# Performance work log

Measured on AMD Instinct MI355X. Metric: run time of the kernel, lower is better.

## Reference

```python
import jax, jax.numpy as jnp
import numpy as np

B, F, T, D, O = 8192, 512, 64, 6, 128
N_INTERNAL = 2 ** D - 1  # 63
N_LEAVES = 2 ** D        # 64


def smooth_step(t):
    tc = jnp.clip(t, -0.5, 0.5)
    return -2.0 * tc ** 3 + 1.5 * tc + 0.5


def setup_inputs() -> dict:
    key = jax.random.key(0)
    k1, k2, k3, k4 = jax.random.split(key, 4)
    x = jax.random.normal(k1, (B, F), dtype=jnp.float32)
    # Stacked per-node Linear weights in BFS (heap) order: node i -> row i.
    W_nodes = jax.random.normal(k2, (N_INTERNAL, F, T), dtype=jnp.float32) * (1.0 / np.sqrt(F))
    b_nodes = jax.random.normal(k3, (N_INTERNAL, T), dtype=jnp.float32) * 0.01
    # Per-leaf mixing weight [out_features, num_trees], leaves in BFS order.
    W_leaf = jax.random.normal(k4, (N_LEAVES, O, T), dtype=jnp.float32)
    return {"x": x, "W_nodes": W_nodes, "b_nodes": b_nodes, "W_leaf": W_leaf}


def reference(x, W_nodes, b_nodes, W_leaf):
    n_internal = W_nodes.shape[0]
    depth = int(np.log2(n_internal + 1))
    # All internal-node gates in one stacked GEMM: [B, n_internal, T]
    s = smooth_step(jnp.einsum('bf,nft->bnt', x, W_nodes) + b_nodes[None, :, :])
    b, _, t = s.shape
    prob = jnp.ones((b, 1, t), dtype=s.dtype)  # root prob
    start = 0
    for lvl in range(depth):
        width = 2 ** lvl
        s_l = s[:, start:start + width]  # [B, width, T], nodes at this level
        start += width
        # node local j -> children local 2j (left, prob*s) and 2j+1 (right, prob*(1-s))
        prob = jnp.stack([prob * s_l, prob * (1.0 - s_l)], axis=2).reshape(b, 2 * width, t)
    # prob: [B, n_leaves, T]; mix per-leaf, per-tree weights -> [B, O]
    out = jnp.einsum('blt,lot->bo', prob, W_leaf)
    return out
```

## Files before the change

### kernel.cpp

```cpp
#include <hip/hip_runtime.h>
#include <hip/hip_fp16.h>

#define BATCH 8192
#define FDIM  512
#define NTREE 64
#define NODES 63
#define ODIM  128
#define NJP   4096
#define K2    4096
#define TPG   8

typedef _Float16 f16;
typedef _Float16 f16x2 __attribute__((ext_vector_type(2)));
typedef _Float16 f16x4 __attribute__((ext_vector_type(4)));
typedef _Float16 f16x8 __attribute__((ext_vector_type(8)));
typedef float    f32x4 __attribute__((ext_vector_type(4)));

#define XH_OFF   0
#define XH_SZ    ((size_t)BATCH*FDIM*2)
#define WNH_OFF  (XH_OFF + XH_SZ)
#define WNH_SZ   ((size_t)NJP*FDIM*2)
#define WLT_OFF  (WNH_OFF + WNH_SZ)
#define WLT_SZ   ((size_t)ODIM*K2*2)
#define PS_OFF   (WLT_OFF + WLT_SZ)
#define PS_SZ    ((size_t)TPG*BATCH*ODIM*4)
#define WS_NEEDED (PS_OFF + PS_SZ)

__device__ __forceinline__ float smooth_step_f(float t) {
    float tc = fminf(fmaxf(t, -0.5f), 0.5f);
    return fmaf(tc, fmaf(-2.0f * tc, tc, 1.5f), 0.5f);
}

__device__ __forceinline__ int sw_off(int row, int g) {
    return ((row >> 3) * 512) + (((row & 7) * 8 + (g ^ (row & 7))) * 8);
}

__global__ __launch_bounds__(256)
void prep_kernel(const float* __restrict__ x, const float* __restrict__ wn,
                 const float* __restrict__ wl,
                 f16* __restrict__ xf, f16* __restrict__ wnf, f16* __restrict__ wlf)
{
    const int bid = blockIdx.x, tid = threadIdx.x;
    if (bid < 512) {
        const int bx = bid >> 3, k0 = bid & 7;
        f16* dst = xf + ((size_t)bx * 8192 + (size_t)k0 * 1024) * 8;
        #pragma unroll
        for (int c = 0; c < 4; ++c) {
            int fid  = c * 256 + tid;
            int lane = fid & 63, ks = (fid >> 6) & 1, tm = (fid >> 7) & 3, wm = (fid >> 9) & 1;
            int row  = bx * 128 + wm * 64 + tm * 16 + (lane & 15);
            int k    = k0 * 64 + (ks * 4 + (lane >> 4)) * 8;
            const float* s = x + (size_t)row * FDIM + k;
            float4 a = *(const float4*)s, b = *(const float4*)(s + 4);
            f16x8 v = { (f16)a.x, (f16)a.y, (f16)a.z, (f16)a.w,
                        (f16)b.x, (f16)b.y, (f16)b.z, (f16)b.w };
            *(f16x8*)(dst + (size_t)fid * 8) = v;
        }
    } else if (bid < 768) {
        const int id = bid - 512, tp = id >> 3, k0 = id & 7;
        f16* dst = wnf + ((size_t)tp * 8192 + (size_t)k0 * 1024) * 8;
        #pragma unroll
        for (int c = 0; c < 4; ++c) {
            int fid  = c * 256 + tid;
            int lane = fid & 63, ks = (fid >> 6) & 1, tn = (fid >> 7) & 3, wq = (fid >> 9) & 1;
            int col  = tp * 128 + wq * 64 + tn * 16 + (lane & 15);
            int t    = col >> 6, n = col & 63;
            int k    = k0 * 64 + (ks * 4 + (lane >> 4)) * 8;
            f16x8 v;
            if (n == NODES) {
                #pragma unroll
                for (int e = 0; e < 8; ++e) v[e] = (f16)0.0f;
            } else {
                const float* s = wn + ((size_t)n * FDIM + k) * NTREE + t;
                #pragma unroll
                for (int e = 0; e < 8; ++e) v[e] = (f16)s[(size_t)e * NTREE];
            }
            *(f16x8*)(dst + (size_t)fid * 8) = v;
        }
    } else {
        const int tp = bid - 768;
        f16* dst = wlf + (size_t)tp * 2048 * 8;
        #pragma unroll
        for (int c = 0; c < 8; ++c) {
            int fid  = c * 256 + tid;
            int lane = fid & 63, ks = (fid >> 6) & 1, tn = (fid >> 7) & 3, wq = (fid >> 9) & 1;
            int h    = (fid >> 10) & 1;
            int o    = wq * 64 + tn * 16 + (lane & 15);
            int t    = tp * 2 + h;
            int l0   = (ks * 4 + (lane >> 4)) * 8;
            const float* s = wl + ((size_t)l0 * ODIM + o) * NTREE + t;
            f16x8 v;
            #pragma unroll
            for (int e = 0; e < 8; ++e) v[e] = (f16)s[(size_t)e * ODIM * NTREE];
            *(f16x8*)(dst + (size_t)fid * 8) = v;
        }
    }
}

__global__ __launch_bounds__(256, 2)
void fused_tree(const f16* __restrict__ xhF, const f16* __restrict__ wnhF,
                const float* __restrict__ bn, const f16* __restrict__ wltF,
                float* __restrict__ partial)
{
    __shared__ __align__(16) f16 SH[16640];
    const int tid  = threadIdx.x;
    const int lane = tid & 63;
    const int w    = tid >> 6;
    const int wm   = w & 1;
    const int wq   = w >> 1;
    const int row0 = blockIdx.x * 128;
    const int tpg  = blockIdx.y;

    const int frow = tid & 127;
    const int ftr  = tid >> 7;

    const f16x8* __restrict__ xv = (const f16x8*)xhF;
    const f16x8* __restrict__ wv = (const f16x8*)wnhF;
    const f16x8* __restrict__ lv = (const f16x8*)wltF;
    const size_t xb = (size_t)blockIdx.x * 8192 + (size_t)wm * 512 + lane;

    f32x4 lacc[4][4] = {};

    for (int tpi = 0; tpi < 4; ++tpi) {
        const int tp = tpg * 4 + tpi;
        const int j0 = tp * 128;

        const size_t wb = (size_t)tp * 8192 + (size_t)wq * 512 + lane;
        f32x4 acc[4][4] = {};
        #pragma unroll 2
        for (int k0 = 0; k0 < 8; ++k0) {
            #pragma unroll
            for (int ks = 0; ks < 2; ++ks) {
                f16x8 bfr[4];
                #pragma unroll
                for (int tn = 0; tn < 4; ++tn)
                    bfr[tn] = wv[wb + k0 * 1024 + tn * 128 + ks * 64];
                #pragma unroll
                for (int tm = 0; tm < 4; ++tm) {
                    f16x8 afr = xv[xb + k0 * 1024 + tm * 128 + ks * 64];
                    #pragma unroll
                    for (int tn = 0; tn < 4; ++tn)
                        acc[tm][tn] = __builtin_amdgcn_mfma_f32_16x16x32_f16(afr, bfr[tn], acc[tm][tn], 0, 0, 0);
                }
            }
        }

        #pragma unroll
        for (int tn = 0; tn < 4; ++tn) {
            int col = wq * 64 + tn * 16 + (lane & 15);
            int nn  = col & 63;
            int tt  = (j0 + col) >> 6;
            float bias = (nn < NODES) ? bn[nn * NTREE + tt] : 0.0f;
            #pragma unroll
            for (int tm = 0; tm < 4; ++tm) {
                #pragma unroll
                for (int r = 0; r < 4; ++r) {
                    int row = wm * 64 + tm * 16 + (lane >> 4) * 4 + r;
                    SH[row * 130 + col] = (f16)smooth_step_f(acc[tm][tn][r] + bias);
                }
            }
        }
        __syncthreads();

        f16x8 ov[8];
        {
            const f16* gp = &SH[frow * 130 + ftr * 64];
            float gg[64];
            #pragma unroll
            for (int c = 0; c < 32; ++c) {
                f16x2 v = *(const f16x2*)(gp + 2 * c);
                gg[2 * c]     = (float)v[0];
                gg[2 * c + 1] = (float)v[1];
            }
            __syncthreads();
            float pr[32];
            pr[0] = 1.0f;
            int bse = 0;
            #pragma unroll
            for (int lvl = 0; lvl < 5; ++lvl) {
                const int width = 1 << lvl;
                #pragma unroll
                for (int i = width - 1; i >= 0; --i) {
                    float p = pr[i], s = gg[bse + i];
                    pr[2 * i]     = p * s;
                    pr[2 * i + 1] = p * (1.0f - s);
                }
                bse += width;
            }
            #pragma unroll
            for (int i = 0; i < 32; ++i) {
                float s5 = gg[31 + i];
                float p  = pr[i];
                ov[i >> 2][(i & 3) * 2]     = (f16)(p * s5);
                ov[i >> 2][(i & 3) * 2 + 1] = (f16)(p * (1.0f - s5));
            }
        }

        #pragma unroll
        for (int g2 = 0; g2 < 8; ++g2)
            *(f16x8*)&SH[ftr * 8192 + sw_off(frow, g2)] = ov[g2];
        __syncthreads();

        const size_t lb = (size_t)tp * 2048 + (size_t)wq * 512 + lane;
        #pragma unroll
        for (int h = 0; h < 2; ++h) {
            #pragma unroll
            for (int ks = 0; ks < 2; ++ks) {
                int g = ks * 4 + (lane >> 4);
                f16x8 bfr[4];
                #pragma unroll
                for (int tn = 0; tn < 4; ++tn)
                    bfr[tn] = lv[lb + h * 1024 + tn * 128 + ks * 64];
                #pragma unroll
                for (int tm = 0; tm < 4; ++tm) {
                    int m = wm * 64 + tm * 16 + (lane & 15);
                    f16x8 afr = *(const f16x8*)&SH[h * 8192 + sw_off(m, g)];
                    #pragma unroll
                    for (int tn = 0; tn < 4; ++tn)
                        lacc[tm][tn] = __builtin_amdgcn_mfma_f32_16x16x32_f16(afr, bfr[tn], lacc[tm][tn], 0, 0, 0);
                }
            }
        }
        __syncthreads();
    }

    float* dst = partial + (size_t)tpg * BATCH * ODIM;
    #pragma unroll
    for (int tn = 0; tn < 4; ++tn) {
        int o = wq * 64 + tn * 16 + (lane & 15);
        #pragma unroll
        for (int tm = 0; tm < 4; ++tm) {
            #pragma unroll
            for (int r = 0; r < 4; ++r) {
                int row = row0 + wm * 64 + tm * 16 + (lane >> 4) * 4 + r;
                dst[(size_t)row * ODIM + o] = lacc[tm][tn][r];
            }
        }
    }
}

__global__ void reduce_kernel(const float* __restrict__ partial, float* __restrict__ out) {
    size_t i = ((size_t)blockIdx.x * blockDim.x + threadIdx.x) * 4;
    f32x4 a = *(const f32x4*)(partial + i);
    #pragma unroll
    for (int k = 1; k < TPG; ++k)
        a += *(const f32x4*)(partial + (size_t)k * BATCH * ODIM + i);
    *(f32x4*)(out + i) = a;
}

#define ROWS 8
__global__ __launch_bounds__(256, 2)
void soft_tree_fallback(const float* __restrict__ x, const float* __restrict__ Wn,
                        const float* __restrict__ bn, const float* __restrict__ Wl,
                        float* __restrict__ out)
{
    __shared__ __half s_lds[ROWS][NODES][NTREE];
    const int lane = threadIdx.x & 63;
    const int w    = threadIdx.x >> 6;
    const long row0 = (long)blockIdx.x * ROWS;
    for (int n = w; n < NODES; n += 4) {
        const float* wp = Wn + ((long)n * FDIM) * NTREE + lane;
        const float* xp = x + row0 * FDIM;
        float acc[ROWS];
        #pragma unroll
        for (int r = 0; r < ROWS; ++r) acc[r] = 0.0f;
        #pragma unroll 8
        for (int f = 0; f < FDIM; ++f) {
            float wv = wp[(long)f * NTREE];
            #pragma unroll
            for (int r = 0; r < ROWS; ++r)
                acc[r] = fmaf(xp[r * FDIM + f], wv, acc[r]);
        }
        float bias = bn[n * NTREE + lane];
        #pragma unroll
        for (int r = 0; r < ROWS; ++r)
            s_lds[r][n][lane] = __float2half(smooth_step_f(acc[r] + bias));
    }
    __syncthreads();
    const int r0 = w * 2, r1 = w * 2 + 1;
    float pr0[64], pr1[64];
    {
        pr0[0] = 1.0f; pr1[0] = 1.0f;
        int base = 0;
        #pragma unroll
        for (int lvl = 0; lvl < 6; ++lvl) {
            const int width = 1 << lvl;
            #pragma unroll
            for (int i = width - 1; i >= 0; --i) {
                float sa = __half2float(s_lds[r0][base + i][lane]);
                float sb = __half2float(s_lds[r1][base + i][lane]);
                float pa = pr0[i], pb = pr1[i];
                pr0[2 * i] = pa * sa; pr0[2 * i + 1] = pa * (1.0f - sa);
                pr1[2 * i] = pb * sb; pr1[2 * i + 1] = pb * (1.0f - sb);
            }
            base += width;
        }
    }
    for (int o = 0; o < ODIM; ++o) {
        const float* wlp = Wl + (long)o * NTREE + lane;
        float c0 = 0.0f, c1 = 0.0f;
        #pragma unroll
        for (int l = 0; l < 64; ++l) {
            float wv = wlp[(long)l * (ODIM * NTREE)];
            c0 = fmaf(pr0[l], wv, c0);
            c1 = fmaf(pr1[l], wv, c1);
        }
        #pragma unroll
        for (int off = 32; off > 0; off >>= 1) {
            c0 += __shfl_xor(c0, off, 64);
            c1 += __shfl_xor(c1, off, 64);
        }
        if (lane == 0) {
            out[(row0 + r0) * ODIM + o] = c0;
            out[(row0 + r1) * ODIM + o] = c1;
        }
    }
}

extern "C" void kernel_launch(void* const* d_in, const int* in_sizes, int n_in,
                              void* d_out, int out_size, void* d_ws, size_t ws_size,
                              hipStream_t stream) {
    const float* x  = (const float*)d_in[0];
    const float* Wn = (const float*)d_in[1];
    const float* bn = (const float*)d_in[2];
    const float* Wl = (const float*)d_in[3];
    float* out = (float*)d_out;

    if (ws_size < WS_NEEDED) {
        soft_tree_fallback<<<BATCH / ROWS, 256, 0, stream>>>(x, Wn, bn, Wl, out);
        return;
    }

    f16*   xh  = (f16*)((char*)d_ws + XH_OFF);
    f16*   wnh = (f16*)((char*)d_ws + WNH_OFF);
    f16*   wlt = (f16*)((char*)d_ws + WLT_OFF);
    float* ps  = (float*)((char*)d_ws + PS_OFF);

    prep_kernel<<<800, 256, 0, stream>>>(x, Wn, Wl, xh, wnh, wlt);
    fused_tree<<<dim3(BATCH / 128, TPG), 256, 0, stream>>>(xh, wnh, bn, wlt, ps);
    reduce_kernel<<<(BATCH * ODIM) / (256 * 4), 256, 0, stream>>>(ps, out);
}
```

Baseline: 161.8 us.

## Halve fused tree block rows, split leaf-prob work, coalesce weight prep reads

The fused tree kernel now handles 64 batch rows per block instead of 128, which halves the accumulator registers and raises launch bounds to four blocks per CU. That doubles the grid and gives more parallelism. The leaf-probability stage is split so two threads share each row-tree pair, each computing half the subtree and reading gates straight from shared memory. The gates and leaf tiles are kept in separate LDS regions, so one barrier is dropped. Prep kernels for the node and leaf weights now read float4 along the tree dimension for coalesced loads, with a changed block count, at the cost of reloading node weights twice as often across the doubled grid.

```diff
diff --git a/kernel.cpp b/kernel.cpp
--- a/kernel.cpp
+++ b/kernel.cpp
@@ -47,8 +47,8 @@
         #pragma unroll
         for (int c = 0; c < 4; ++c) {
             int fid  = c * 256 + tid;
-            int lane = fid & 63, ks = (fid >> 6) & 1, tm = (fid >> 7) & 3, wm = (fid >> 9) & 1;
-            int row  = bx * 128 + wm * 64 + tm * 16 + (lane & 15);
+            int lane = fid & 63, ks = (fid >> 6) & 1, rg = (fid >> 7) & 7;
+            int row  = bx * 128 + rg * 16 + (lane & 15);
             int k    = k0 * 64 + (ks * 4 + (lane >> 4)) * 8;
             const float* s = x + (size_t)row * FDIM + k;
             float4 a = *(const float4*)s, b = *(const float4*)(s + 4);
@@ -57,76 +57,89 @@
             *(f16x8*)(dst + (size_t)fid * 8) = v;
         }
     } else if (bid < 768) {
-        const int id = bid - 512, tp = id >> 3, k0 = id & 7;
-        f16* dst = wnf + ((size_t)tp * 8192 + (size_t)k0 * 1024) * 8;
-        #pragma unroll
-        for (int c = 0; c < 4; ++c) {
-            int fid  = c * 256 + tid;
-            int lane = fid & 63, ks = (fid >> 6) & 1, tn = (fid >> 7) & 3, wq = (fid >> 9) & 1;
-            int col  = tp * 128 + wq * 64 + tn * 16 + (lane & 15);
-            int t    = col >> 6, n = col & 63;
-            int k    = k0 * 64 + (ks * 4 + (lane >> 4)) * 8;
+        const int id = bid - 512;
+        const int t0 = (id >> 4) * 4;
+        const int n  = tid & 63;
+        const int k8 = (id & 15) * 4 + (tid >> 6);
+        float4 q[8];
+        if (n != NODES) {
+            #pragma unroll
+            for (int e = 0; e < 8; ++e)
+                q[e] = *(const float4*)(wn + ((size_t)n * FDIM + k8 * 8 + e) * NTREE + t0);
+        }
+        #pragma unroll
+        for (int j = 0; j < 4; ++j) {
+            int t  = t0 + j;
+            int tp = t >> 1;
+            int cg = (t & 1) * 4 + (n >> 4);
+            size_t chunk = (size_t)tp * 8192 + (size_t)(k8 >> 3) * 1024 + cg * 128
+                         + ((k8 >> 2) & 1) * 64 + (k8 & 3) * 16 + (n & 15);
             f16x8 v;
             if (n == NODES) {
                 #pragma unroll
                 for (int e = 0; e < 8; ++e) v[e] = (f16)0.0f;
             } else {
-                const float* s = wn + ((size_t)n * FDIM + k) * NTREE + t;
-                #pragma unroll
-                for (int e = 0; e < 8; ++e) v[e] = (f16)s[(size_t)e * NTREE];
-            }
-            *(f16x8*)(dst + (size_t)fid * 8) = v;
+                const float* qf = (const float*)q;
+                #pragma unroll
+                for (int e = 0; e < 8; ++e) v[e] = (f16)qf[e * 4 + j];
+            }
+            *(f16x8*)(wnf + chunk * 8) = v;
         }
     } else {
-        const int tp = bid - 768;
-        f16* dst = wlf + (size_t)tp * 2048 * 8;
-        #pragma unroll
-        for (int c = 0; c < 8; ++c) {
-            int fid  = c * 256 + tid;
-            int lane = fid & 63, ks = (fid >> 6) & 1, tn = (fid >> 7) & 3, wq = (fid >> 9) & 1;
-            int h    = (fid >> 10) & 1;
-            int o    = wq * 64 + tn * 16 + (lane & 15);
-            int t    = tp * 2 + h;
-            int l0   = (ks * 4 + (lane >> 4)) * 8;
-            const float* s = wl + ((size_t)l0 * ODIM + o) * NTREE + t;
+        const int id = bid - 768;
+        const int t0 = (id >> 2) * 4;
+        const int o  = tid & 127;
+        const int l8 = (id & 3) * 2 + (tid >> 7);
+        float4 q[8];
+        #pragma unroll
+        for (int e = 0; e < 8; ++e)
+            q[e] = *(const float4*)(wl + ((size_t)(l8 * 8 + e) * ODIM + o) * NTREE + t0);
+        #pragma unroll
+        for (int j = 0; j < 4; ++j) {
+            int t  = t0 + j;
+            int tp = t >> 1, h = t & 1;
+            size_t chunk = (size_t)tp * 2048 + (size_t)h * 1024 + (o >> 4) * 128
+                         + (l8 >> 2) * 64 + (l8 & 3) * 16 + (o & 15);
+            const float* qf = (const float*)q;
             f16x8 v;
             #pragma unroll
-            for (int e = 0; e < 8; ++e) v[e] = (f16)s[(size_t)e * ODIM * NTREE];
-            *(f16x8*)(dst + (size_t)fid * 8) = v;
-        }
-    }
-}
-
-__global__ __launch_bounds__(256, 2)
+            for (int e = 0; e < 8; ++e) v[e] = (f16)qf[e * 4 + j];
+            *(f16x8*)(wlf + chunk * 8) = v;
+        }
+    }
+}
+
+__global__ __launch_bounds__(256, 4)
 void fused_tree(const f16* __restrict__ xhF, const f16* __restrict__ wnhF,
                 const float* __restrict__ bn, const f16* __restrict__ wltF,
                 float* __restrict__ partial)
 {
-    __shared__ __align__(16) f16 SH[16640];
+    __shared__ __align__(16) f16 SH[16512];
     const int tid  = threadIdx.x;
     const int lane = tid & 63;
     const int w    = tid >> 6;
     const int wm   = w & 1;
     const int wq   = w >> 1;
-    const int row0 = blockIdx.x * 128;
     const int tpg  = blockIdx.y;
 
-    const int frow = tid & 127;
-    const int ftr  = tid >> 7;
+    const int frow = tid & 63;
+    const int ftr  = (tid >> 6) & 1;
+    const int sub  = tid >> 7;
 
     const f16x8* __restrict__ xv = (const f16x8*)xhF;
     const f16x8* __restrict__ wv = (const f16x8*)wnhF;
     const f16x8* __restrict__ lv = (const f16x8*)wltF;
-    const size_t xb = (size_t)blockIdx.x * 8192 + (size_t)wm * 512 + lane;
-
-    f32x4 lacc[4][4] = {};
+    const size_t xb = (size_t)(blockIdx.x >> 1) * 8192
+                    + (size_t)((blockIdx.x & 1) * 4 + wm * 2) * 128 + lane;
+
+    f32x4 lacc[2][4] = {};
 
     for (int tpi = 0; tpi < 4; ++tpi) {
         const int tp = tpg * 4 + tpi;
         const int j0 = tp * 128;
 
         const size_t wb = (size_t)tp * 8192 + (size_t)wq * 512 + lane;
-        f32x4 acc[4][4] = {};
+        f32x4 acc[2][4] = {};
         #pragma unroll 2
         for (int k0 = 0; k0 < 8; ++k0) {
             #pragma unroll
@@ -136,7 +149,7 @@
                 for (int tn = 0; tn < 4; ++tn)
                     bfr[tn] = wv[wb + k0 * 1024 + tn * 128 + ks * 64];
                 #pragma unroll
-                for (int tm = 0; tm < 4; ++tm) {
+                for (int tm = 0; tm < 2; ++tm) {
                     f16x8 afr = xv[xb + k0 * 1024 + tm * 128 + ks * 64];
                     #pragma unroll
                     for (int tn = 0; tn < 4; ++tn)
@@ -152,53 +165,53 @@
             int tt  = (j0 + col) >> 6;
             float bias = (nn < NODES) ? bn[nn * NTREE + tt] : 0.0f;
             #pragma unroll
-            for (int tm = 0; tm < 4; ++tm) {
+            for (int tm = 0; tm < 2; ++tm) {
                 #pragma unroll
                 for (int r = 0; r < 4; ++r) {
-                    int row = wm * 64 + tm * 16 + (lane >> 4) * 4 + r;
+                    int row = wm * 32 + tm * 16 + (lane >> 4) * 4 + r;
                     SH[row * 130 + col] = (f16)smooth_step_f(acc[tm][tn][r] + bias);
                 }
             }
         }
         __syncthreads();
 
-        f16x8 ov[8];
         {
             const f16* gp = &SH[frow * 130 + ftr * 64];
-            float gg[64];
-            #pragma unroll
-            for (int c = 0; c < 32; ++c) {
-                f16x2 v = *(const f16x2*)(gp + 2 * c);
-                gg[2 * c]     = (float)v[0];
-                gg[2 * c + 1] = (float)v[1];
-            }
-            __syncthreads();
-            float pr[32];
-            pr[0] = 1.0f;
-            int bse = 0;
-            #pragma unroll
-            for (int lvl = 0; lvl < 5; ++lvl) {
-                const int width = 1 << lvl;
-                #pragma unroll
-                for (int i = width - 1; i >= 0; --i) {
-                    float p = pr[i], s = gg[bse + i];
-                    pr[2 * i]     = p * s;
-                    pr[2 * i + 1] = p * (1.0f - s);
-                }
-                bse += width;
-            }
-            #pragma unroll
-            for (int i = 0; i < 32; ++i) {
-                float s5 = gg[31 + i];
-                float p  = pr[i];
-                ov[i >> 2][(i & 3) * 2]     = (f16)(p * s5);
-                ov[i >> 2][(i & 3) * 2 + 1] = (f16)(p * (1.0f - s5));
-            }
-        }
-
-        #pragma unroll
-        for (int g2 = 0; g2 < 8; ++g2)
-            *(f16x8*)&SH[ftr * 8192 + sw_off(frow, g2)] = ov[g2];
+            float pq[16];
+            {
+                float g0 = (float)gp[0];
+                float p  = sub ? 1.0f - g0 : g0;
+                float s1 = (float)gp[1 + sub];
+                pq[0] = p * s1; pq[1] = p * (1.0f - s1);
+                #pragma unroll
+                for (int m = 1; m >= 0; --m) {
+                    float s = (float)gp[3 + sub * 2 + m]; float pp = pq[m];
+                    pq[2 * m] = pp * s; pq[2 * m + 1] = pp * (1.0f - s);
+                }
+                #pragma unroll
+                for (int m = 3; m >= 0; --m) {
+                    float s = (float)gp[7 + sub * 4 + m]; float pp = pq[m];
+                    pq[2 * m] = pp * s; pq[2 * m + 1] = pp * (1.0f - s);
+                }
+                #pragma unroll
+                for (int m = 7; m >= 0; --m) {
+                    float s = (float)gp[15 + sub * 8 + m]; float pp = pq[m];
+                    pq[2 * m] = pp * s; pq[2 * m + 1] = pp * (1.0f - s);
+                }
+            }
+            f16x8 ov[4];
+            #pragma unroll
+            for (int ii = 0; ii < 16; ++ii) {
+                float s5 = (float)gp[31 + sub * 16 + ii];
+                float p  = pq[ii];
+                int ll   = 2 * ii;
+                ov[ll >> 3][ll & 7]       = (f16)(p * s5);
+                ov[ll >> 3][(ll & 7) + 1] = (f16)(p * (1.0f - s5));
+            }
+            #pragma unroll
+            for (int q = 0; q < 4; ++q)
+                *(f16x8*)&SH[8320 + ftr * 4096 + sw_off(frow, sub * 4 + q)] = ov[q];
+        }
         __syncthreads();
 
         const size_t lb = (size_t)tp * 2048 + (size_t)wq * 512 + lane;
@@ -212,9 +225,9 @@
                 for (int tn = 0; tn < 4; ++tn)
                     bfr[tn] = lv[lb + h * 1024 + tn * 128 + ks * 64];
                 #pragma unroll
-                for (int tm = 0; tm < 4; ++tm) {
-                    int m = wm * 64 + tm * 16 + (lane & 15);
-                    f16x8 afr = *(const f16x8*)&SH[h * 8192 + sw_off(m, g)];
+                for (int tm = 0; tm < 2; ++tm) {
+                    int m = wm * 32 + tm * 16 + (lane & 15);
+                    f16x8 afr = *(const f16x8*)&SH[8320 + h * 4096 + sw_off(m, g)];
                     #pragma unroll
                     for (int tn = 0; tn < 4; ++tn)
                         lacc[tm][tn] = __builtin_amdgcn_mfma_f32_16x16x32_f16(afr, bfr[tn], lacc[tm][tn], 0, 0, 0);
@@ -225,14 +238,15 @@
     }
 
     float* dst = partial + (size_t)tpg * BATCH * ODIM;
+    const int row0 = blockIdx.x * 64;
     #pragma unroll
     for (int tn = 0; tn < 4; ++tn) {
         int o = wq * 64 + tn * 16 + (lane & 15);
         #pragma unroll
-        for (int tm = 0; tm < 4; ++tm) {
+        for (int tm = 0; tm < 2; ++tm) {
             #pragma unroll
             for (int r = 0; r < 4; ++r) {
-                int row = row0 + wm * 64 + tm * 16 + (lane >> 4) * 4 + r;
+                int row = row0 + wm * 32 + tm * 16 + (lane >> 4) * 4 + r;
                 dst[(size_t)row * ODIM + o] = lacc[tm][tn][r];
             }
         }
@@ -336,7 +350,7 @@
     f16*   wlt = (f16*)((char*)d_ws + WLT_OFF);
     float* ps  = (float*)((char*)d_ws + PS_OFF);
 
-    prep_kernel<<<800, 256, 0, stream>>>(x, Wn, Wl, xh, wnh, wlt);
-    fused_tree<<<dim3(BATCH / 128, TPG), 256, 0, stream>>>(xh, wnh, bn, wlt, ps);
+    prep_kernel<<<832, 256, 0, stream>>>(x, Wn, Wl, xh, wnh, wlt);
+    fused_tree<<<dim3(BATCH / 64, TPG), 256, 0, stream>>>(xh, wnh, bn, wlt, ps);
     reduce_kernel<<<(BATCH * ODIM) / (256 * 4), 256, 0, stream>>>(ps, out);
 }
```

Measured after the change: 154.0 us. 4.8% less time.

## Fuse partial-sum reduction into tree kernel and vectorize weight repacking

Applied to the files above, without the earlier changes.

The separate reduce kernel is removed. Each fused_tree block now bumps a per-row-block atomic counter after writing its partial, and the last of the TPG blocks for a row block sums all partials and writes the output. The counter is zeroed by an extra block in prep_kernel. The weight-repacking branches of prep_kernel are also rewritten to load float4 runs along the tree dimension instead of strided scalar loads, with the output index computed accordingly. This removes one kernel launch and improves coalescing of the weight reads, at the cost of a fence plus atomic in every block and a serialized tail reduction.

```diff
diff --git a/kernel.cpp b/kernel.cpp
--- a/kernel.cpp
+++ b/kernel.cpp
@@ -24,7 +24,9 @@
 #define WLT_SZ   ((size_t)ODIM*K2*2)
 #define PS_OFF   (WLT_OFF + WLT_SZ)
 #define PS_SZ    ((size_t)TPG*BATCH*ODIM*4)
-#define WS_NEEDED (PS_OFF + PS_SZ)
+#define CNT_OFF  (PS_OFF + PS_SZ)
+#define CNT_SZ   ((size_t)4096)
+#define WS_NEEDED (CNT_OFF + CNT_SZ)
 
 __device__ __forceinline__ float smooth_step_f(float t) {
     float tc = fminf(fmaxf(t, -0.5f), 0.5f);
@@ -38,17 +40,22 @@
 __global__ __launch_bounds__(256)
 void prep_kernel(const float* __restrict__ x, const float* __restrict__ wn,
                  const float* __restrict__ wl,
-                 f16* __restrict__ xf, f16* __restrict__ wnf, f16* __restrict__ wlf)
+                 f16* __restrict__ xf, f16* __restrict__ wnf, f16* __restrict__ wlf,
+                 int* __restrict__ cnt)
 {
     const int bid = blockIdx.x, tid = threadIdx.x;
+    if (bid == 832) {
+        if (tid < 64) cnt[tid] = 0;
+        return;
+    }
     if (bid < 512) {
         const int bx = bid >> 3, k0 = bid & 7;
         f16* dst = xf + ((size_t)bx * 8192 + (size_t)k0 * 1024) * 8;
         #pragma unroll
         for (int c = 0; c < 4; ++c) {
             int fid  = c * 256 + tid;
-            int lane = fid & 63, ks = (fid >> 6) & 1, tm = (fid >> 7) & 3, wm = (fid >> 9) & 1;
-            int row  = bx * 128 + wm * 64 + tm * 16 + (lane & 15);
+            int lane = fid & 63, ks = (fid >> 6) & 1, rg = (fid >> 7) & 7;
+            int row  = bx * 128 + rg * 16 + (lane & 15);
             int k    = k0 * 64 + (ks * 4 + (lane >> 4)) * 8;
             const float* s = x + (size_t)row * FDIM + k;
             float4 a = *(const float4*)s, b = *(const float4*)(s + 4);
@@ -57,42 +64,54 @@
             *(f16x8*)(dst + (size_t)fid * 8) = v;
         }
     } else if (bid < 768) {
-        const int id = bid - 512, tp = id >> 3, k0 = id & 7;
-        f16* dst = wnf + ((size_t)tp * 8192 + (size_t)k0 * 1024) * 8;
-        #pragma unroll
-        for (int c = 0; c < 4; ++c) {
-            int fid  = c * 256 + tid;
-            int lane = fid & 63, ks = (fid >> 6) & 1, tn = (fid >> 7) & 3, wq = (fid >> 9) & 1;
-            int col  = tp * 128 + wq * 64 + tn * 16 + (lane & 15);
-            int t    = col >> 6, n = col & 63;
-            int k    = k0 * 64 + (ks * 4 + (lane >> 4)) * 8;
+        const int id = bid - 512;
+        const int t0 = (id >> 4) * 4;
+        const int n  = tid & 63;
+        const int k8 = (id & 15) * 4 + (tid >> 6);
+        float4 q[8];
+        if (n != NODES) {
+            #pragma unroll
+            for (int e = 0; e < 8; ++e)
+                q[e] = *(const float4*)(wn + ((size_t)n * FDIM + k8 * 8 + e) * NTREE + t0);
+        }
+        #pragma unroll
+        for (int j = 0; j < 4; ++j) {
+            int t  = t0 + j;
+            int tp = t >> 1;
+            int cg = (t & 1) * 4 + (n >> 4);
+            size_t chunk = (size_t)tp * 8192 + (size_t)(k8 >> 3) * 1024 + cg * 128
+                         + ((k8 >> 2) & 1) * 64 + (k8 & 3) * 16 + (n & 15);
             f16x8 v;
             if (n == NODES) {
                 #pragma unroll
                 for (int e = 0; e < 8; ++e) v[e] = (f16)0.0f;
             } else {
-                const float* s = wn + ((size_t)n * FDIM + k) * NTREE + t;
-                #pragma unroll
-                for (int e = 0; e < 8; ++e) v[e] = (f16)s[(size_t)e * NTREE];
-            }
-            *(f16x8*)(dst + (size_t)fid * 8) = v;
+                const float* qf = (const float*)q;
+                #pragma unroll
+                for (int e = 0; e < 8; ++e) v[e] = (f16)qf[e * 4 + j];
+            }
+            *(f16x8*)(wnf + chunk * 8) = v;
         }
     } else {
-        const int tp = bid - 768;
-        f16* dst = wlf + (size_t)tp * 2048 * 8;
-        #pragma unroll
-        for (int c = 0; c < 8; ++c) {
-            int fid  = c * 256 + tid;
-            int lane = fid & 63, ks = (fid >> 6) & 1, tn = (fid >> 7) & 3, wq = (fid >> 9) & 1;
-            int h    = (fid >> 10) & 1;
-            int o    = wq * 64 + tn * 16 + (lane & 15);
-            int t    = tp * 2 + h;
-            int l0   = (ks * 4 + (lane >> 4)) * 8;
-            const float* s = wl + ((size_t)l0 * ODIM + o) * NTREE + t;
+        const int id = bid - 768;
+        const int t0 = (id >> 2) * 4;
+        const int o  = tid & 127;
+        const int l8 = (id & 3) * 2 + (tid >> 7);
+        float4 q[8];
+        #pragma unroll
+        for (int e = 0; e < 8; ++e)
+            q[e] = *(const float4*)(wl + ((size_t)(l8 * 8 + e) * ODIM + o) * NTREE + t0);
+        #pragma unroll
+        for (int j = 0; j < 4; ++j) {
+            int t  = t0 + j;
+            int tp = t >> 1, h = t & 1;
+            size_t chunk = (size_t)tp * 2048 + (size_t)h * 1024 + (o >> 4) * 128
+                         + (l8 >> 2) * 64 + (l8 & 3) * 16 + (o & 15);
+            const float* qf = (const float*)q;
             f16x8 v;
             #pragma unroll
-            for (int e = 0; e < 8; ++e) v[e] = (f16)s[(size_t)e * ODIM * NTREE];
-            *(f16x8*)(dst + (size_t)fid * 8) = v;
+            for (int e = 0; e < 8; ++e) v[e] = (f16)qf[e * 4 + j];
+            *(f16x8*)(wlf + chunk * 8) = v;
         }
     }
 }
@@ -100,9 +119,11 @@
 __global__ __launch_bounds__(256, 2)
 void fused_tree(const f16* __restrict__ xhF, const f16* __restrict__ wnhF,
                 const float* __restrict__ bn, const f16* __restrict__ wltF,
-                float* __restrict__ partial)
+                float* __restrict__ partial, float* __restrict__ out,
+                int* __restrict__ cnt)
 {
     __shared__ __align__(16) f16 SH[16640];
+    __shared__ int s_last;
     const int tid  = threadIdx.x;
     const int lane = tid & 63;
     const int w    = tid >> 6;
@@ -237,15 +258,24 @@
             }
         }
     }
-}
-
-__global__ void reduce_kernel(const float* __restrict__ partial, float* __restrict__ out) {
-    size_t i = ((size_t)blockIdx.x * blockDim.x + threadIdx.x) * 4;
-    f32x4 a = *(const f32x4*)(partial + i);
-    #pragma unroll
-    for (int k = 1; k < TPG; ++k)
-        a += *(const f32x4*)(partial + (size_t)k * BATCH * ODIM + i);
-    *(f32x4*)(out + i) = a;
+
+    __threadfence();
+    if (tid == 0)
+        s_last = (atomicAdd(cnt + blockIdx.x, 1) == TPG - 1);
+    __syncthreads();
+    if (s_last) {
+        __threadfence();
+        const size_t rb = (size_t)row0 * ODIM;
+        #pragma unroll
+        for (int c = 0; c < 16; ++c) {
+            size_t idx = rb + ((size_t)c * 256 + tid) * 4;
+            f32x4 a = *(const f32x4*)(partial + idx);
+            #pragma unroll
+            for (int k = 1; k < TPG; ++k)
+                a += *(const f32x4*)(partial + (size_t)k * BATCH * ODIM + idx);
+            *(f32x4*)(out + idx) = a;
+        }
+    }
 }
 
 #define ROWS 8
@@ -335,8 +365,8 @@
     f16*   wnh = (f16*)((char*)d_ws + WNH_OFF);
     f16*   wlt = (f16*)((char*)d_ws + WLT_OFF);
     float* ps  = (float*)((char*)d_ws + PS_OFF);
-
-    prep_kernel<<<800, 256, 0, stream>>>(x, Wn, Wl, xh, wnh, wlt);
-    fused_tree<<<dim3(BATCH / 128, TPG), 256, 0, stream>>>(xh, wnh, bn, wlt, ps);
-    reduce_kernel<<<(BATCH * ODIM) / (256 * 4), 256, 0, stream>>>(ps, out);
-}
+    int*   cnt = (int*)((char*)d_ws + CNT_OFF);
+
+    prep_kernel<<<833, 256, 0, stream>>>(x, Wn, Wl, xh, wnh, wlt, cnt);
+    fused_tree<<<dim3(BATCH / 128, TPG), 256, 0, stream>>>(xh, wnh, bn, wlt, ps, out, cnt);
+}
```

After: 218.8 us. +35.2%, slower.
